# Performance work log

Measured on AMD Instinct MI355X. Metric: run time of the kernel, lower is better.

The kernel has to match this reference:

```python
import jax, jax.numpy as jnp
import numpy as np

D_MODEL = 768
N_HEADS = 12
D_K = D_MODEL // N_HEADS
NEG_INF = -1e10


def setup_inputs() -> dict:
    key = jax.random.key(0)
    ks = jax.random.split(key, 12)
    B, S = 2, 4096
    scale = 1.0 / np.sqrt(D_MODEL)
    inp = {
        "q": jax.random.normal(ks[0], (B, S, D_MODEL), jnp.float32),
        "k": jax.random.normal(ks[1], (B, S, D_MODEL), jnp.float32),
        "v": jax.random.normal(ks[2], (B, S, D_MODEL), jnp.float32),
        "mask": jnp.ones((B, S), jnp.int32),
        "Wq": jax.random.normal(ks[3], (D_MODEL, D_MODEL), jnp.float32) * scale,
        "bq": jnp.zeros((D_MODEL,), jnp.float32),
        "Wk": jax.random.normal(ks[4], (D_MODEL, D_MODEL), jnp.float32) * scale,
        "bk": jnp.zeros((D_MODEL,), jnp.float32),
        "Wv": jax.random.normal(ks[5], (D_MODEL, D_MODEL), jnp.float32) * scale,
        "bv": jnp.zeros((D_MODEL,), jnp.float32),
        "Wo": jax.random.normal(ks[6], (D_MODEL, D_MODEL), jnp.float32) * scale,
        "bo": jnp.zeros((D_MODEL,), jnp.float32),
    }
    return inp


def reference(q, k, v, mask, Wq, bq, Wk, bk, Wv, bv, Wo, bo):
    B, Sq, _ = q.shape
    Sk = k.shape[1]
    # linear projections (flax Linear: x @ kernel + bias)
    query = q @ Wq + bq
    key_ = k @ Wk + bk
    value = v @ Wv + bv
    # split heads: [B, H, S, d_k]
    query = query.reshape(B, Sq, N_HEADS, D_K).transpose(0, 2, 1, 3)
    key_ = key_.reshape(B, Sk, N_HEADS, D_K).transpose(0, 2, 1, 3)
    value = value.reshape(B, Sk, N_HEADS, D_K).transpose(0, 2, 1, 3)
    # scores [B, H, Sq, Sk]
    scores = jnp.einsum('bhqd,bhkd->bhqk', query, key_) / jnp.sqrt(
        jnp.asarray(D_K, query.dtype))
    m = mask[:, None, None, :]  # 2D mask -> [B,1,1,Sk]
    scores = jnp.where(m == 0, NEG_INF, scores)
    attn = jax.nn.softmax(scores, axis=-1)
    # dropout deterministic (is_training=False): identity
    x = jnp.einsum('bhqk,bhkd->bhqd', attn, value)
    x = x.transpose(0, 2, 1, 3).reshape(B, Sq, D_MODEL)
    return x @ Wo + bo
```

## Files before the change

kernel.cpp:

```cpp
#include <hip/hip_runtime.h>

typedef __attribute__((ext_vector_type(8))) short short8;
typedef __attribute__((ext_vector_type(4))) float floatx4;
typedef __attribute__((ext_vector_type(16))) float floatx16;
typedef unsigned short ushort_t;

#define S_LEN 4096
#define NH 12
#define DK 64
#define DM 768
#define BQ 128
#define LOG2E 1.4426950408889634f

static __device__ __forceinline__ unsigned short f2bf(float f) {
    unsigned int u = __float_as_uint(f);
    u += 0x7FFFu + ((u >> 16) & 1u);
    return (unsigned short)(u >> 16);
}
static __device__ __forceinline__ unsigned pack2(float a, float b) {
    return (unsigned)f2bf(a) | ((unsigned)f2bf(b) << 16);
}

__global__ __launch_bounds__(256)
void wtrans_kernel(const float* __restrict__ W0, const float* __restrict__ W1,
                   const float* __restrict__ W2, const float* __restrict__ W3,
                   ushort_t* __restrict__ T0, ushort_t* __restrict__ T1,
                   ushort_t* __restrict__ T2, ushort_t* __restrict__ T3) {
    __shared__ float tile[32][33];
    const int z = blockIdx.z;
    const float* W = (z == 0) ? W0 : (z == 1) ? W1 : (z == 2) ? W2 : W3;
    ushort_t* T = (z == 0) ? T0 : (z == 1) ? T1 : (z == 2) ? T2 : T3;
    const int bx = blockIdx.x, by = blockIdx.y;
    const int tx = threadIdx.x, ty = threadIdx.y;
    #pragma unroll
    for (int j = 0; j < 32; j += 8)
        tile[ty + j][tx] = W[(size_t)(by * 32 + ty + j) * DM + bx * 32 + tx];
    __syncthreads();
    #pragma unroll
    for (int j = 0; j < 32; j += 8)
        T[(size_t)(bx * 32 + ty + j) * DM + by * 32 + tx] = f2bf(tile[tx][ty + j]);
}

__global__ __launch_bounds__(256)
void cvt_kernel(const float* __restrict__ A0, const float* __restrict__ A1,
                const float* __restrict__ A2, ushort_t* __restrict__ O0,
                ushort_t* __restrict__ O1, ushort_t* __restrict__ O2) {
    const int z = blockIdx.y;
    const float* A = (z == 0) ? A0 : (z == 1) ? A1 : A2;
    ushort_t* O = (z == 0) ? O0 : (z == 1) ? O1 : O2;
    const size_t i = ((size_t)blockIdx.x * 256 + threadIdx.x) * 8;
    const float4 f0 = *(const float4*)(A + i);
    const float4 f1 = *(const float4*)(A + i + 4);
    uint4 o;
    o.x = pack2(f0.x, f0.y);
    o.y = pack2(f0.z, f0.w);
    o.z = pack2(f1.x, f1.y);
    o.w = pack2(f1.z, f1.w);
    *(uint4*)(O + i) = o;
}

__global__ __launch_bounds__(256)
void vtrans_kernel(const ushort_t* __restrict__ Vn, ushort_t* __restrict__ Vt) {
    __shared__ ushort_t tl[64 * 72];
    const int s0 = blockIdx.x * 64;
    const size_t bh = blockIdx.y;
    const int t = threadIdx.x;
    {
        const int r = t >> 2, c0 = (t & 3) * 16;
        const uint4* src = (const uint4*)(Vn + (bh * S_LEN + s0 + r) * DK + c0);
        uint4 a0 = src[0], a1 = src[1];
        uint4* dst = (uint4*)&tl[r * 72 + c0];
        dst[0] = a0;
        dst[1] = a1;
    }
    __syncthreads();
    {
        const int d = t >> 2, c0 = (t & 3) * 16;
        alignas(16) ushort_t tmp[16];
        #pragma unroll
        for (int j = 0; j < 16; ++j) tmp[j] = tl[(c0 + j) * 72 + d];
        uint4* dst = (uint4*)(Vt + (bh * DK + d) * S_LEN + s0 + c0);
        dst[0] = *(const uint4*)&tmp[0];
        dst[1] = *(const uint4*)&tmp[8];
    }
}

struct GemmArgs {
    const ushort_t* A[3];
    const ushort_t* Wt[3];
    const float* bias[3];
    void* C[3];
    float scale[3];
};

template <int MODE>
__global__ __launch_bounds__(256, 2)
void gemm_kernel(GemmArgs args) {
    __shared__ ushort_t As[128 * 40];
    __shared__ ushort_t Bs[128 * 40];
    const int z = blockIdx.z;
    const ushort_t* A = args.A[z];
    const ushort_t* Wt = args.Wt[z];
    const float* bias = args.bias[z];
    void* Carg = args.C[z];
    const float scale = args.scale[z];

    const int m0 = blockIdx.x * 128;
    const int n0 = blockIdx.y * 128;
    const int t = threadIdx.x;
    const int r = t >> 1;
    const int half = t & 1;
    const int w = t >> 6, lane = t & 63, l15 = lane & 15, quad = lane >> 4;
    const int rowoff = (w >> 1) * 64, coloff = (w & 1) * 64;

    floatx4 acc[4][4];
    #pragma unroll
    for (int i = 0; i < 4; ++i)
        #pragma unroll
        for (int j = 0; j < 4; ++j) acc[i][j] = (floatx4){0.f, 0.f, 0.f, 0.f};

    for (int kt = 0; kt < DM; kt += 32) {
        __syncthreads();
        {
            const uint4* src = (const uint4*)(A + (size_t)(m0 + r) * DM + kt + half * 16);
            uint4 a0 = src[0], a1 = src[1];
            uint4* dst = (uint4*)&As[r * 40 + half * 16];
            dst[0] = a0;
            dst[1] = a1;
        }
        {
            const uint4* src = (const uint4*)(Wt + (size_t)(n0 + r) * DM + kt + half * 16);
            uint4 b0 = src[0], b1 = src[1];
            uint4* dst = (uint4*)&Bs[r * 40 + half * 16];
            dst[0] = b0;
            dst[1] = b1;
        }
        __syncthreads();
        short8 af[4], bfr[4];
        #pragma unroll
        for (int i = 0; i < 4; ++i)
            af[i] = *(const short8*)&As[(rowoff + 16 * i + l15) * 40 + quad * 8];
        #pragma unroll
        for (int j = 0; j < 4; ++j)
            bfr[j] = *(const short8*)&Bs[(coloff + 16 * j + l15) * 40 + quad * 8];
        #pragma unroll
        for (int i = 0; i < 4; ++i)
            #pragma unroll
            for (int j = 0; j < 4; ++j)
                acc[i][j] = __builtin_amdgcn_mfma_f32_16x16x32_bf16(af[i], bfr[j], acc[i][j], 0, 0, 0);
    }

    #pragma unroll
    for (int i = 0; i < 4; ++i) {
        #pragma unroll
        for (int j = 0; j < 4; ++j) {
            #pragma unroll
            for (int reg = 0; reg < 4; ++reg) {
                const int m = m0 + rowoff + 16 * i + quad * 4 + reg;
                const int n = n0 + coloff + 16 * j + l15;
                const float v2 = (acc[i][j][reg] + bias[n]) * scale;
                if (MODE == 0) {
                    ushort_t* Out = (ushort_t*)Carg;
                    const int b = m >> 12, s = m & 4095, h = n >> 6, d = n & 63;
                    Out[((size_t)((b * NH + h) * S_LEN + s)) * DK + d] = f2bf(v2);
                } else {
                    float* Out = (float*)Carg;
                    Out[(size_t)m * DM + n] = v2;
                }
            }
        }
    }
}

__global__ __launch_bounds__(256, 3)
void attn_kernel(const ushort_t* __restrict__ Q, const ushort_t* __restrict__ K,
                 const ushort_t* __restrict__ VT, const int* __restrict__ mask,
                 ushort_t* __restrict__ X) {
    __shared__ ushort_t Qs[BQ * DK];
    __shared__ ushort_t Ks[2][64 * DK];
    __shared__ ushort_t Vs[2][64 * DK];

    const int id = blockIdx.x;
    const int per = id >> 3;
    const int bh = (id & 7) * 3 + (per >> 5);
    const int qb = per & 31;
    const int b = bh / NH, h = bh - b * NH;
    const size_t bho = (size_t)bh * S_LEN;
    const ushort_t* Vbase = VT + (size_t)bh * DK * S_LEN;
    const int t = threadIdx.x;
    const int w = t >> 6, lane = t & 63, l31 = lane & 31, half = lane >> 5;
    const int q0 = qb * BQ;
    const int swl = l31 & 7;

    {
        const int r = t >> 1;
        #pragma unroll
        for (int i = 0; i < 4; ++i) {
            const int c8 = (t & 1) * 4 + i;
            uint4 a = *(const uint4*)(Q + (bho + q0 + r) * DK + c8 * 8);
            *(uint4*)&Qs[r * DK + ((c8 ^ (r & 7)) << 3)] = a;
        }
    }
    const int sr = t >> 2;
    const int sc0 = (t & 3) * 2;
    {
        uint4 k0 = *(const uint4*)(K + (bho + sr) * DK + sc0 * 8);
        uint4 k1 = *(const uint4*)(K + (bho + sr) * DK + sc0 * 8 + 8);
        uint4 v0 = *(const uint4*)(Vbase + (size_t)sr * S_LEN + sc0 * 8);
        uint4 v1 = *(const uint4*)(Vbase + (size_t)sr * S_LEN + sc0 * 8 + 8);
        *(uint4*)&Ks[0][sr * DK + ((sc0 ^ (sr & 7)) << 3)] = k0;
        *(uint4*)&Ks[0][sr * DK + (((sc0 + 1) ^ (sr & 7)) << 3)] = k1;
        *(uint4*)&Vs[0][sr * DK + ((sc0 ^ (sr & 7)) << 3)] = v0;
        *(uint4*)&Vs[0][sr * DK + (((sc0 + 1) ^ (sr & 7)) << 3)] = v1;
    }
    __syncthreads();

    short8 qf[4];
    #pragma unroll
    for (int ks = 0; ks < 4; ++ks) {
        const int row = w * 32 + l31;
        const int c8 = ks * 2 + half;
        qf[ks] = *(const short8*)&Qs[row * DK + ((c8 ^ swl) << 3)];
    }
    ushort_t* Ps = &Qs[(w * 32) * DK];

    floatx16 o[2];
    #pragma unroll
    for (int dt = 0; dt < 2; ++dt)
        #pragma unroll
        for (int r = 0; r < 16; ++r) o[dt][r] = 0.f;
    float l_r = 0.f;

    for (int it = 0; it < S_LEN / 64; ++it) {
        const int cur = it & 1;
        __syncthreads();
        const bool hn = (it + 1 < S_LEN / 64);
        uint4 k0n, k1n, v0n, v1n;
        if (hn) {
            const int kvn = (it + 1) * 64;
            k0n = *(const uint4*)(K + (bho + kvn + sr) * DK + sc0 * 8);
            k1n = *(const uint4*)(K + (bho + kvn + sr) * DK + sc0 * 8 + 8);
            v0n = *(const uint4*)(Vbase + (size_t)sr * S_LEN + kvn + sc0 * 8);
            v1n = *(const uint4*)(Vbase + (size_t)sr * S_LEN + kvn + sc0 * 8 + 8);
        }
        const int mv = mask[(size_t)b * S_LEN + it * 64 + lane];
        const unsigned long long mb = __ballot(mv != 0);

        const ushort_t* Kc = Ks[cur];
        const ushort_t* Vc = Vs[cur];

        floatx16 st[2];
        #pragma unroll
        for (int kt = 0; kt < 2; ++kt) {
            floatx16 s;
            #pragma unroll
            for (int r = 0; r < 16; ++r) s[r] = 0.f;
            #pragma unroll
            for (int ks = 0; ks < 4; ++ks) {
                const int c8 = ks * 2 + half;
                const short8 kf = *(const short8*)&Kc[(kt * 32 + l31) * DK + ((c8 ^ swl) << 3)];
                s = __builtin_amdgcn_mfma_f32_32x32x16_bf16(kf, qf[ks], s, 0, 0, 0);
            }
            st[kt] = s;
        }

        if (mb != ~0ULL) {
            #pragma unroll
            for (int kt = 0; kt < 2; ++kt) {
                const unsigned bits = (unsigned)(mb >> (kt * 32));
                const unsigned vbits = bits >> (half * 4);
                #pragma unroll
                for (int r = 0; r < 16; ++r)
                    if (!((vbits >> ((r & 3) + 8 * (r >> 2))) & 1)) st[kt][r] = -3.0e10f;
            }
        }

        #pragma unroll
        for (int kt = 0; kt < 2; ++kt) {
            #pragma unroll
            for (int g = 0; g < 4; ++g) {
                const float p0 = __builtin_amdgcn_exp2f(st[kt][g * 4 + 0]);
                const float p1 = __builtin_amdgcn_exp2f(st[kt][g * 4 + 1]);
                const float p2 = __builtin_amdgcn_exp2f(st[kt][g * 4 + 2]);
                const float p3 = __builtin_amdgcn_exp2f(st[kt][g * 4 + 3]);
                l_r += (p0 + p1) + (p2 + p3);
                const int c8 = kt * 4 + g;
                uint2 pk;
                pk.x = pack2(p0, p1);
                pk.y = pack2(p2, p3);
                *(uint2*)&Ps[l31 * DK + ((c8 ^ swl) << 3) + half * 4] = pk;
            }
        }
        __asm__ __volatile__("" ::: "memory");

        short8 pf[4];
        #pragma unroll
        for (int ks = 0; ks < 4; ++ks) {
            const int c8 = ks * 2 + half;
            pf[ks] = *(const short8*)&Ps[l31 * DK + ((c8 ^ swl) << 3)];
        }
        #pragma unroll
        for (int dt = 0; dt < 2; ++dt) {
            #pragma unroll
            for (int ks = 0; ks < 4; ++ks) {
                const int c8 = ks * 2 + half;
                const short8 vf = *(const short8*)&Vc[(dt * 32 + l31) * DK + ((c8 ^ swl) << 3)];
                o[dt] = __builtin_amdgcn_mfma_f32_32x32x16_bf16(pf[ks], vf, o[dt], 0, 0, 0);
            }
        }

        if (hn) {
            *(uint4*)&Ks[1 - cur][sr * DK + ((sc0 ^ (sr & 7)) << 3)] = k0n;
            *(uint4*)&Ks[1 - cur][sr * DK + (((sc0 + 1) ^ (sr & 7)) << 3)] = k1n;
            *(uint4*)&Vs[1 - cur][sr * DK + ((sc0 ^ (sr & 7)) << 3)] = v0n;
            *(uint4*)&Vs[1 - cur][sr * DK + (((sc0 + 1) ^ (sr & 7)) << 3)] = v1n;
        }
    }

    l_r += __shfl_xor(l_r, 32);
    const float inv = 1.0f / l_r;
    float iv[16];
    #pragma unroll
    for (int r = 0; r < 16; ++r)
        iv[r] = __shfl(inv, (r & 3) + 8 * (r >> 2) + 4 * half);
    #pragma unroll
    for (int dt = 0; dt < 2; ++dt)
        #pragma unroll
        for (int r = 0; r < 16; ++r) {
            const int qrow = (r & 3) + 8 * (r >> 2) + 4 * half;
            const int s = q0 + w * 32 + qrow;
            const int d = h * DK + dt * 32 + l31;
            X[((size_t)b * S_LEN + s) * DM + d] = f2bf(o[dt][r] * iv[r]);
        }
}

extern "C" void kernel_launch(void* const* d_in, const int* in_sizes, int n_in,
                              void* d_out, int out_size, void* d_ws, size_t ws_size,
                              hipStream_t stream) {
    const float* q = (const float*)d_in[0];
    const float* k = (const float*)d_in[1];
    const float* v = (const float*)d_in[2];
    const int* mask = (const int*)d_in[3];
    const float* Wq = (const float*)d_in[4];
    const float* bq = (const float*)d_in[5];
    const float* Wk = (const float*)d_in[6];
    const float* bk = (const float*)d_in[7];
    const float* Wv = (const float*)d_in[8];
    const float* bv = (const float*)d_in[9];
    const float* Wo = (const float*)d_in[10];
    const float* bo = (const float*)d_in[11];
    float* out = (float*)d_out;

    const size_t ME = (size_t)2 * S_LEN * DM;
    const size_t WE = (size_t)DM * DM;
    ushort_t* Qb = (ushort_t*)d_ws;
    ushort_t* Kb = Qb + ME;
    ushort_t* Vb = Kb + ME;
    ushort_t* VTb = Vb + ME;
    ushort_t* Xb = VTb + ME;
    ushort_t* Wqt = Xb + ME;
    ushort_t* Wkt = Wqt + WE;
    ushort_t* Wvt = Wkt + WE;
    ushort_t* Wot = Wvt + WE;
    ushort_t* Qa = Xb;
    ushort_t* Ka = VTb;
    ushort_t* Va = (ushort_t*)d_out;

    wtrans_kernel<<<dim3(DM / 32, DM / 32, 4), dim3(32, 8), 0, stream>>>(
        Wq, Wk, Wv, Wo, Wqt, Wkt, Wvt, Wot);

    cvt_kernel<<<dim3((int)(ME / 8 / 256), 3), 256, 0, stream>>>(q, k, v, Qa, Ka, Va);

    GemmArgs g1;
    g1.A[0] = Qa;  g1.A[1] = Ka;  g1.A[2] = Va;
    g1.Wt[0] = Wqt; g1.Wt[1] = Wkt; g1.Wt[2] = Wvt;
    g1.bias[0] = bq; g1.bias[1] = bk; g1.bias[2] = bv;
    g1.C[0] = Qb;  g1.C[1] = Kb;  g1.C[2] = Vb;
    g1.scale[0] = 0.125f * LOG2E;
    g1.scale[1] = 1.0f; g1.scale[2] = 1.0f;
    gemm_kernel<0><<<dim3((2 * S_LEN) / 128, DM / 128, 3), 256, 0, stream>>>(g1);

    vtrans_kernel<<<dim3(S_LEN / 64, 2 * NH), 256, 0, stream>>>(Vb, VTb);

    attn_kernel<<<dim3(768), 256, 0, stream>>>(Qb, Kb, VTb, mask, Xb);

    GemmArgs g2;
    g2.A[0] = Xb;  g2.A[1] = Xb;  g2.A[2] = Xb;
    g2.Wt[0] = Wot; g2.Wt[1] = Wot; g2.Wt[2] = Wot;
    g2.bias[0] = bo; g2.bias[1] = bo; g2.bias[2] = bo;
    g2.C[0] = out; g2.C[1] = out; g2.C[2] = out;
    g2.scale[0] = 1.0f; g2.scale[1] = 1.0f; g2.scale[2] = 1.0f;
    gemm_kernel<1><<<dim3((2 * S_LEN) / 128, DM / 128, 1), 256, 0, stream>>>(g2);
}
```

Baseline: 364.1 us.

## Use direct global-to-LDS loads in GEMM and attention, precheck mask once

Replaces the register-staged global-to-shared copies in both the projection GEMM and the attention kernel with `global_load_lds` DMA-style loads. In attention the XOR swizzle moves from the LDS destination to the global source address. The double-buffered K/V loop is unrolled by two so buffer pointers are fixed per half. An all-ones mask check is done once per block with `__syncthreads_and`, which skips the per-iteration mask load and ballot. It also switches to a cheaper round-half-up bf16 pack and removes the GEMM shared-memory padding so it can run 3 blocks per SM. The risks are LDS bank conflicts in the unpadded GEMM tiles, and relying on compiler-inserted waits for the async LDS fills in the attention loop.

```diff
diff --git a/kernel.cpp b/kernel.cpp
--- a/kernel.cpp
+++ b/kernel.cpp
@@ -19,6 +19,16 @@
 }
 static __device__ __forceinline__ unsigned pack2(float a, float b) {
     return (unsigned)f2bf(a) | ((unsigned)f2bf(b) << 16);
+}
+static __device__ __forceinline__ unsigned pack2f(float a, float b) {
+    unsigned au = __float_as_uint(a) + 0x8000u;
+    unsigned bu = __float_as_uint(b) + 0x8000u;
+    return (bu & 0xFFFF0000u) | (au >> 16);
+}
+static __device__ __forceinline__ void gld_lds16(const void* g, void* l) {
+    __builtin_amdgcn_global_load_lds(
+        (__attribute__((address_space(1))) void*)g,
+        (__attribute__((address_space(3))) void*)l, 16, 0, 0);
 }
 
 __global__ __launch_bounds__(256)
@@ -94,10 +104,10 @@
 };
 
 template <int MODE>
-__global__ __launch_bounds__(256, 2)
+__global__ __launch_bounds__(256, 3)
 void gemm_kernel(GemmArgs args) {
-    __shared__ ushort_t As[128 * 40];
-    __shared__ ushort_t Bs[128 * 40];
+    __shared__ ushort_t As[128 * 32];
+    __shared__ ushort_t Bs[128 * 32];
     const int z = blockIdx.z;
     const ushort_t* A = args.A[z];
     const ushort_t* Wt = args.Wt[z];
@@ -108,10 +118,10 @@
     const int m0 = blockIdx.x * 128;
     const int n0 = blockIdx.y * 128;
     const int t = threadIdx.x;
-    const int r = t >> 1;
-    const int half = t & 1;
     const int w = t >> 6, lane = t & 63, l15 = lane & 15, quad = lane >> 4;
     const int rowoff = (w >> 1) * 64, coloff = (w & 1) * 64;
+    const int srow = w * 16 + (lane >> 2);
+    const int scol = (lane & 3) * 8;
 
     floatx4 acc[4][4];
     #pragma unroll
@@ -121,28 +131,21 @@
 
     for (int kt = 0; kt < DM; kt += 32) {
         __syncthreads();
-        {
-            const uint4* src = (const uint4*)(A + (size_t)(m0 + r) * DM + kt + half * 16);
-            uint4 a0 = src[0], a1 = src[1];
-            uint4* dst = (uint4*)&As[r * 40 + half * 16];
-            dst[0] = a0;
-            dst[1] = a1;
-        }
-        {
-            const uint4* src = (const uint4*)(Wt + (size_t)(n0 + r) * DM + kt + half * 16);
-            uint4 b0 = src[0], b1 = src[1];
-            uint4* dst = (uint4*)&Bs[r * 40 + half * 16];
-            dst[0] = b0;
-            dst[1] = b1;
-        }
+        #pragma unroll
+        for (int j = 0; j < 2; ++j) {
+            const int r = j * 64 + srow;
+            gld_lds16(A + (size_t)(m0 + r) * DM + kt + scol, &As[r * 32 + scol]);
+            gld_lds16(Wt + (size_t)(n0 + r) * DM + kt + scol, &Bs[r * 32 + scol]);
+        }
+        __asm__ __volatile__("s_waitcnt vmcnt(0)" ::: "memory");
         __syncthreads();
         short8 af[4], bfr[4];
         #pragma unroll
         for (int i = 0; i < 4; ++i)
-            af[i] = *(const short8*)&As[(rowoff + 16 * i + l15) * 40 + quad * 8];
+            af[i] = *(const short8*)&As[(rowoff + 16 * i + l15) * 32 + quad * 8];
         #pragma unroll
         for (int j = 0; j < 4; ++j)
-            bfr[j] = *(const short8*)&Bs[(coloff + 16 * j + l15) * 40 + quad * 8];
+            bfr[j] = *(const short8*)&Bs[(coloff + 16 * j + l15) * 32 + quad * 8];
         #pragma unroll
         for (int i = 0; i < 4; ++i)
             #pragma unroll
@@ -177,8 +180,8 @@
                  const ushort_t* __restrict__ VT, const int* __restrict__ mask,
                  ushort_t* __restrict__ X) {
     __shared__ ushort_t Qs[BQ * DK];
-    __shared__ ushort_t Ks[2][64 * DK];
-    __shared__ ushort_t Vs[2][64 * DK];
+    __shared__ ushort_t Ks0[64 * DK], Ks1[64 * DK];
+    __shared__ ushort_t Vs0[64 * DK], Vs1[64 * DK];
 
     const int id = blockIdx.x;
     const int per = id >> 3;
@@ -191,36 +194,50 @@
     const int w = t >> 6, lane = t & 63, l31 = lane & 31, half = lane >> 5;
     const int q0 = qb * BQ;
     const int swl = l31 & 7;
-
+    const int frow8 = lane >> 3;
+    const int fcc = lane & 7;
+
+    auto fillK = [&](int kv0, ushort_t* Kb) {
+        #pragma unroll
+        for (int j = 0; j < 2; ++j) {
+            const int r = (w * 2 + j) * 8 + frow8;
+            const int c8 = fcc ^ (r & 7);
+            gld_lds16(K + (bho + kv0 + r) * DK + c8 * 8, &Kb[r * DK + fcc * 8]);
+        }
+    };
+    auto fillV = [&](int kv0, ushort_t* Vb) {
+        #pragma unroll
+        for (int j = 0; j < 2; ++j) {
+            const int r = (w * 2 + j) * 8 + frow8;
+            const int c8 = fcc ^ (r & 7);
+            gld_lds16(Vbase + (size_t)r * S_LEN + kv0 + c8 * 8, &Vb[r * DK + fcc * 8]);
+        }
+    };
+
+    fillK(0, Ks0);
+    fillV(0, Vs0);
+    #pragma unroll
+    for (int j = 0; j < 4; ++j) {
+        const int r = (w * 4 + j) * 8 + frow8;
+        const int c8 = fcc ^ (r & 7);
+        gld_lds16(Q + (bho + q0 + r) * DK + c8 * 8, &Qs[r * DK + fcc * 8]);
+    }
+    int ok = 1;
     {
-        const int r = t >> 1;
+        const int* mrow = mask + (size_t)b * S_LEN + t * 16;
         #pragma unroll
         for (int i = 0; i < 4; ++i) {
-            const int c8 = (t & 1) * 4 + i;
-            uint4 a = *(const uint4*)(Q + (bho + q0 + r) * DK + c8 * 8);
-            *(uint4*)&Qs[r * DK + ((c8 ^ (r & 7)) << 3)] = a;
-        }
-    }
-    const int sr = t >> 2;
-    const int sc0 = (t & 3) * 2;
-    {
-        uint4 k0 = *(const uint4*)(K + (bho + sr) * DK + sc0 * 8);
-        uint4 k1 = *(const uint4*)(K + (bho + sr) * DK + sc0 * 8 + 8);
-        uint4 v0 = *(const uint4*)(Vbase + (size_t)sr * S_LEN + sc0 * 8);
-        uint4 v1 = *(const uint4*)(Vbase + (size_t)sr * S_LEN + sc0 * 8 + 8);
-        *(uint4*)&Ks[0][sr * DK + ((sc0 ^ (sr & 7)) << 3)] = k0;
-        *(uint4*)&Ks[0][sr * DK + (((sc0 + 1) ^ (sr & 7)) << 3)] = k1;
-        *(uint4*)&Vs[0][sr * DK + ((sc0 ^ (sr & 7)) << 3)] = v0;
-        *(uint4*)&Vs[0][sr * DK + (((sc0 + 1) ^ (sr & 7)) << 3)] = v1;
-    }
-    __syncthreads();
+            const int4 mm = *(const int4*)(mrow + i * 4);
+            ok &= (mm.x != 0) & (mm.y != 0) & (mm.z != 0) & (mm.w != 0);
+        }
+    }
+    const int allones = __syncthreads_and(ok);
 
     short8 qf[4];
     #pragma unroll
     for (int ks = 0; ks < 4; ++ks) {
-        const int row = w * 32 + l31;
         const int c8 = ks * 2 + half;
-        qf[ks] = *(const short8*)&Qs[row * DK + ((c8 ^ swl) << 3)];
+        qf[ks] = *(const short8*)&Qs[(w * 32 + l31) * DK + ((c8 ^ swl) << 3)];
     }
     ushort_t* Ps = &Qs[(w * 32) * DK];
 
@@ -231,23 +248,18 @@
         for (int r = 0; r < 16; ++r) o[dt][r] = 0.f;
     float l_r = 0.f;
 
-    for (int it = 0; it < S_LEN / 64; ++it) {
-        const int cur = it & 1;
+    auto body = [&](int it, const ushort_t* Kc, const ushort_t* Vc,
+                    ushort_t* Kn, ushort_t* Vn) {
         __syncthreads();
-        const bool hn = (it + 1 < S_LEN / 64);
-        uint4 k0n, k1n, v0n, v1n;
-        if (hn) {
-            const int kvn = (it + 1) * 64;
-            k0n = *(const uint4*)(K + (bho + kvn + sr) * DK + sc0 * 8);
-            k1n = *(const uint4*)(K + (bho + kvn + sr) * DK + sc0 * 8 + 8);
-            v0n = *(const uint4*)(Vbase + (size_t)sr * S_LEN + kvn + sc0 * 8);
-            v1n = *(const uint4*)(Vbase + (size_t)sr * S_LEN + kvn + sc0 * 8 + 8);
-        }
-        const int mv = mask[(size_t)b * S_LEN + it * 64 + lane];
-        const unsigned long long mb = __ballot(mv != 0);
-
-        const ushort_t* Kc = Ks[cur];
-        const ushort_t* Vc = Vs[cur];
+        if (it + 1 < S_LEN / 64) {
+            fillK((it + 1) * 64, Kn);
+            fillV((it + 1) * 64, Vn);
+        }
+        unsigned long long mb = ~0ULL;
+        if (!allones) {
+            const int mv = mask[(size_t)b * S_LEN + it * 64 + lane];
+            mb = __ballot(mv != 0);
+        }
 
         floatx16 st[2];
         #pragma unroll
@@ -286,8 +298,8 @@
                 l_r += (p0 + p1) + (p2 + p3);
                 const int c8 = kt * 4 + g;
                 uint2 pk;
-                pk.x = pack2(p0, p1);
-                pk.y = pack2(p2, p3);
+                pk.x = pack2f(p0, p1);
+                pk.y = pack2f(p2, p3);
                 *(uint2*)&Ps[l31 * DK + ((c8 ^ swl) << 3) + half * 4] = pk;
             }
         }
@@ -308,13 +320,11 @@
                 o[dt] = __builtin_amdgcn_mfma_f32_32x32x16_bf16(pf[ks], vf, o[dt], 0, 0, 0);
             }
         }
-
-        if (hn) {
-            *(uint4*)&Ks[1 - cur][sr * DK + ((sc0 ^ (sr & 7)) << 3)] = k0n;
-            *(uint4*)&Ks[1 - cur][sr * DK + (((sc0 + 1) ^ (sr & 7)) << 3)] = k1n;
-            *(uint4*)&Vs[1 - cur][sr * DK + ((sc0 ^ (sr & 7)) << 3)] = v0n;
-            *(uint4*)&Vs[1 - cur][sr * DK + (((sc0 + 1) ^ (sr & 7)) << 3)] = v1n;
-        }
+    };
+
+    for (int it = 0; it < S_LEN / 64; it += 2) {
+        body(it, Ks0, Vs0, Ks1, Vs1);
+        body(it + 1, Ks1, Vs1, Ks0, Vs0);
     }
 
     l_r += __shfl_xor(l_r, 32);
```

Measured after the change: 348.4 us. -4.3%, faster.
